# Kernel tuning notes

Measured on AMD Instinct MI355X. Metric: run time of the kernel, lower is better.

The kernel has to match this reference:

```python
import jax, jax.numpy as jnp
import numpy as np
from jax import lax

WINDOW_SIZE = 11
SIGMA = 1.5
LEVELS = 5
WEIGHTS = jnp.array([0.0448, 0.2856, 0.3001, 0.2363, 0.1333], dtype=jnp.float32)


def _make_window(ws, channel):
    # 1D gaussian, sigma=1.5, normalized; outer product -> 2D window, tiled per channel
    x = jnp.arange(ws, dtype=jnp.float32) - ws // 2
    g = jnp.exp(-(x * x) / (2.0 * SIGMA * SIGMA))
    g = g / g.sum()
    w2 = jnp.outer(g, g)  # [ws, ws]
    return jnp.broadcast_to(w2[None, None], (channel, 1, ws, ws))


def _dwconv(x, win, channel):
    # depthwise VALID conv, matches F.conv2d(..., padding=0, groups=channel)
    return lax.conv_general_dilated(
        x, win, window_strides=(1, 1), padding='VALID',
        feature_group_count=channel,
        dimension_numbers=('NCHW', 'OIHW', 'NCHW'))


def _ssim_cs(img1, img2):
    # dynamic data range, as in the torch source (L=1 for [0,1) inputs)
    max_val = jnp.where(jnp.max(img1) > 128.0, 255.0, 1.0)
    min_val = jnp.where(jnp.min(img1) < -0.5, -1.0, 0.0)
    L = max_val - min_val

    n, c, h, w = img1.shape
    ws = min(WINDOW_SIZE, h, w)  # static python int
    win = _make_window(ws, c)

    mu1 = _dwconv(img1, win, c)
    mu2 = _dwconv(img2, win, c)
    mu1_sq = mu1 * mu1
    mu2_sq = mu2 * mu2
    mu1_mu2 = mu1 * mu2
    sigma1_sq = _dwconv(img1 * img1, win, c) - mu1_sq
    sigma2_sq = _dwconv(img2 * img2, win, c) - mu2_sq
    sigma12 = _dwconv(img1 * img2, win, c) - mu1_mu2

    C1 = (0.01 * L) ** 2
    C2 = (0.03 * L) ** 2
    v1 = 2.0 * sigma12 + C2
    v2 = sigma1_sq + sigma2_sq + C2
    cs = jnp.mean(v1 / v2)
    ssim_map = (2.0 * mu1_mu2 + C1) * v1 / ((mu1_sq + mu2_sq + C1) * v2)
    return jnp.mean(ssim_map), cs


def _avg_pool2(x):
    # F.avg_pool2d(x, (2,2)): stride 2, no padding (floors odd dims)
    n, c, h, w = x.shape
    x = x[:, :, : (h // 2) * 2, : (w // 2) * 2]
    return x.reshape(n, c, h // 2, 2, w // 2, 2).mean(axis=(3, 5))


def setup_inputs() -> dict:
    key = jax.random.key(0)
    k1, k2 = jax.random.split(key)
    img1 = jax.random.uniform(k1, (16, 3, 512, 512), dtype=jnp.float32)
    img2 = jax.random.uniform(k2, (16, 3, 512, 512), dtype=jnp.float32)
    return {"img1": img1, "img2": img2}


def reference(img1, img2):
    mssim, mcs = [], []
    for _ in range(LEVELS):  # fixed 5-level pyramid, shapes shrink each level
        s, c = _ssim_cs(img1, img2)
        mssim.append(s)
        mcs.append(c)
        img1 = _avg_pool2(img1)
        img2 = _avg_pool2(img2)
    mssim = (jnp.stack(mssim) + 1.0) / 2.0  # normalize=True
    mcs = (jnp.stack(mcs) + 1.0) / 2.0
    pow1 = mcs ** WEIGHTS
    pow2 = mssim ** WEIGHTS
    # NOTE: faithful to source: prod over (pow1[:-1] * pow2[-1]) broadcasts pow2[-1]
    return jnp.prod(pow1[:-1] * pow2[-1])
```

## Files before the change

kernel.cpp:

```cpp
#include <hip/hip_runtime.h>


#define NSLOT 32

typedef float v4  __attribute__((ext_vector_type(4)));
typedef float v2f __attribute__((ext_vector_type(2)));

__device__ __forceinline__ float frcp(float x) { return __builtin_amdgcn_rcpf(x); }

template<int TROWS, int NTHR, int MINW>
__global__ __launch_bounds__(NTHR, MINW) void ssim_tile_kernel(
    const float* __restrict__ img1, const float* __restrict__ img2,
    float* __restrict__ ds1, float* __restrict__ ds2,
    int H, int do_ds, float* __restrict__ acc)
{
    constexpr int HR    = TROWS + 10;
    constexpr int OPT   = TROWS * 32 / NTHR;
    constexpr int PITCH = 33;
    constexpr int NW    = NTHR / 64;

    const float GW[11] = {0.00102840f, 0.00759877f, 0.03600070f, 0.10936069f,
                          0.21300636f, 0.26601172f, 0.21300636f, 0.10936069f,
                          0.03600070f, 0.00759877f, 0.00102840f};
    const float C1 = 1e-4f, C2 = 9e-4f;

    __shared__ v4 hb[HR * PITCH];
    __shared__ float red[2 * NW];

    const int tid  = threadIdx.x;
    const int nc   = blockIdx.z;
    const int tx0  = blockIdx.x * 32;
    const int ty0  = blockIdx.y * TROWS;
    const int outHW = H - 10;
    const float* p1 = img1 + (size_t)nc * H * H;
    const float* p2 = img2 + (size_t)nc * H * H;

    if (do_ds) {
        const int H2 = H >> 1;
        #pragma unroll
        for (int t = tid; t < 16 * (TROWS / 2); t += NTHR) {
            int r = t >> 4, cdd = t & 15;
            int iy = ty0 + 2 * r, ix = tx0 + 2 * cdd;
            if (iy + 1 < H) {
                v2f a0 = *(const v2f*)(p1 + (size_t)iy * H + ix);
                v2f a1 = *(const v2f*)(p1 + (size_t)(iy + 1) * H + ix);
                v2f b0 = *(const v2f*)(p2 + (size_t)iy * H + ix);
                v2f b1 = *(const v2f*)(p2 + (size_t)(iy + 1) * H + ix);
                size_t o = (size_t)nc * H2 * H2
                         + (size_t)((ty0 >> 1) + r) * H2 + ((tx0 >> 1) + cdd);
                ds1[o] = 0.25f * ((a0.x + a0.y) + (a1.x + a1.y));
                ds2[o] = 0.25f * ((b0.x + b0.y) + (b1.x + b1.y));
            }
        }
    }

    for (int task = tid; task < HR * 8; task += NTHR) {
        const int r  = task >> 3, cg = task & 7;
        const int gr = ty0 + r;
        const int c0 = tx0 + cg * 4;
        v4 hs = 0.f, hd = 0.f, hss = 0.f, hdd = 0.f;
        if (gr < H) {
            float s[16], d[16];
            if (c0 + 16 <= H) {
                const float* pa = p1 + (size_t)gr * H + c0;
                const float* pb = p2 + (size_t)gr * H + c0;
                #pragma unroll
                for (int q = 0; q < 4; ++q) {
                    v4 va = *(const v4*)(pa + 4 * q);
                    v4 vb = *(const v4*)(pb + 4 * q);
                    v4 sv = va + vb, dv = va - vb;
                    s[4*q+0] = sv.x; s[4*q+1] = sv.y; s[4*q+2] = sv.z; s[4*q+3] = sv.w;
                    d[4*q+0] = dv.x; d[4*q+1] = dv.y; d[4*q+2] = dv.z; d[4*q+3] = dv.w;
                }
            } else {
                #pragma unroll
                for (int q = 0; q < 16; ++q) {
                    int cc = c0 + q;
                    float a = (cc < H) ? p1[(size_t)gr * H + cc] : 0.f;
                    float b = (cc < H) ? p2[(size_t)gr * H + cc] : 0.f;
                    s[q] = a + b; d[q] = a - b;
                }
            }
            #pragma unroll
            for (int j = 0; j < 11; ++j) {
                float w = GW[j];
                v4 sv = {s[j], s[j+1], s[j+2], s[j+3]};
                v4 dv = {d[j], d[j+1], d[j+2], d[j+3]};
                v4 ws = w * sv, wd = w * dv;
                hs += ws; hd += wd; hss += ws * sv; hdd += wd * dv;
            }
        }
        v4* row = &hb[r * PITCH + cg * 4];
        row[0] = (v4){hs.x, hd.x, hss.x, hdd.x};
        row[1] = (v4){hs.y, hd.y, hss.y, hdd.y};
        row[2] = (v4){hs.z, hd.z, hss.z, hdd.z};
        row[3] = (v4){hs.w, hd.w, hss.w, hdd.w};
    }
    __syncthreads();

    const int col  = tid & 31;
    const int row0 = (tid >> 5) * OPT;
    const float colm = (tx0 + col < outHW) ? 1.f : 0.f;
    v4 A[OPT];
    #pragma unroll
    for (int k = 0; k < OPT; ++k) A[k] = 0.f;

    #pragma unroll
    for (int r = 0; r < OPT + 10; ++r) {
        v4 h = hb[(row0 + r) * PITCH + col];
        #pragma unroll
        for (int k = 0; k < OPT; ++k) {
            const int j = r - k;
            if (j >= 0 && j < 11) A[k] += GW[j] * h;
        }
    }

    float ssim_t = 0.f, cs_t = 0.f;
    #pragma unroll
    for (int k = 0; k < OPT; ++k) {
        float mask = colm * ((ty0 + row0 + k < outHW) ? 1.f : 0.f);
        float mu_s = A[k].x, mu_d = A[k].y;
        float P = mu_s * mu_s, Q = mu_d * mu_d;
        float U = A[k].z - P, V = A[k].w - Q;
        float v1 = 0.5f * (U - V) + C2;
        float v2 = 0.5f * (U + V) + C2;
        float n1 = 0.5f * (P - Q) + C1;
        float d1 = 0.5f * (P + Q) + C1;
        float csv = v1 * frcp(v2);
        float ssv = n1 * csv * frcp(d1);
        cs_t   += mask * csv;
        ssim_t += mask * ssv;
    }

    #pragma unroll
    for (int off = 32; off > 0; off >>= 1) {
        ssim_t += __shfl_down(ssim_t, off);
        cs_t   += __shfl_down(cs_t, off);
    }
    int wave = tid >> 6, lane = tid & 63;
    if (lane == 0) { red[wave] = ssim_t; red[NW + wave] = cs_t; }
    __syncthreads();
    if (tid == 0) {
        float s = 0.f, c2s = 0.f;
        #pragma unroll
        for (int w = 0; w < NW; ++w) { s += red[w]; c2s += red[NW + w]; }
        int slot = (blockIdx.x + blockIdx.y * 5 + blockIdx.z * 11) & (NSLOT - 1);
        atomicAdd(&acc[slot], s);
        atomicAdd(&acc[NSLOT + slot], c2s);
    }
}

__global__ void finalize_kernel(const float* __restrict__ acc, float* __restrict__ out)
{
    if (threadIdx.x == 0 && blockIdx.x == 0) {
        const float w[5] = {0.0448f, 0.2856f, 0.3001f, 0.2363f, 0.1333f};
        float ms[5], mc[5];
        for (int l = 0; l < 5; ++l) {
            float s = 0.f, c = 0.f;
            for (int k = 0; k < NSLOT; ++k) {
                s += acc[2 * NSLOT * l + k];
                c += acc[2 * NSLOT * l + NSLOT + k];
            }
            int oh = (512 >> l) - 10;
            float cnt = 48.f * (float)oh * (float)oh;
            ms[l] = (s / cnt + 1.f) * 0.5f;
            mc[l] = (c / cnt + 1.f) * 0.5f;
        }
        float p2 = powf(ms[4], w[4]);
        float r = 1.f;
        for (int i = 0; i < 4; ++i) r *= powf(mc[i], w[i]) * p2;
        out[0] = r;
    }
}

extern "C" void kernel_launch(void* const* d_in, const int* in_sizes, int n_in,
                              void* d_out, int out_size, void* d_ws, size_t ws_size,
                              hipStream_t stream)
{
    const float* img1 = (const float*)d_in[0];
    const float* img2 = (const float*)d_in[1];
    float* out = (float*)d_out;
    float* ws  = (float*)d_ws;

    float* acc = ws;
    size_t off = 512;

    const float* buf1[5];
    const float* buf2[5];
    float* wbuf1[5];
    float* wbuf2[5];
    buf1[0] = img1; buf2[0] = img2;
    for (int l = 1; l < 5; ++l) {
        int Hl = 512 >> l;
        size_t sz = (size_t)48 * Hl * Hl;
        wbuf1[l] = ws + off; off += sz;
        wbuf2[l] = ws + off; off += sz;
        buf1[l] = wbuf1[l];
        buf2[l] = wbuf2[l];
    }

    hipMemsetAsync(acc, 0, 5 * 2 * NSLOT * sizeof(float), stream);

    const int Hs[5] = {512, 256, 128, 64, 32};
    const int Ts[5] = {64, 64, 32, 16, 16};

    for (int l = 0; l < 5; ++l) {
        int H = Hs[l], T = Ts[l];
        int outH = H - 10;
        int ctiles = (outH + 31) / 32;
        int rtiles = (outH + T - 1) / T;
        dim3 grid(ctiles, rtiles, 48);
        float* d1 = l < 4 ? wbuf1[l + 1] : nullptr;
        float* d2 = l < 4 ? wbuf2[l + 1] : nullptr;
        int dd = l < 4 ? 1 : 0;
        float* a = acc + 2 * NSLOT * l;
        if (T == 64)
            ssim_tile_kernel<64, 512, 8><<<grid, 512, 0, stream>>>(buf1[l], buf2[l], d1, d2, H, dd, a);
        else if (T == 32)
            ssim_tile_kernel<32, 256, 7><<<grid, 256, 0, stream>>>(buf1[l], buf2[l], d1, d2, H, dd, a);
        else
            ssim_tile_kernel<16, 256, 8><<<grid, 256, 0, stream>>>(buf1[l], buf2[l], d1, d2, H, dd, a);
    }

    finalize_kernel<<<1, 64, 0, stream>>>(acc, out);
}
```

Before: 242.9 us.

## Build full pyramid in level-0 kernel and merge coarse levels into one launch

The level-0 kernel now computes every downsampled pyramid level (2x,4x,8x,16x) straight from the full-resolution input tile, and levels 1-4 run as one flattened tail kernel instead of four separate launches. Atomics and the memset are replaced by per-block partial sums that a 512-thread finalize kernel reduces. This removes launch overhead and serialization across the small coarse levels, and drops atomic contention. In exchange, the level-0 blocks do extra uncoalesced recursive pooling reads, and the coarse levels now run at 512 threads with small tiles, which may leave many threads idle.

```diff
diff --git a/kernel.cpp b/kernel.cpp
--- a/kernel.cpp
+++ b/kernel.cpp
@@ -1,18 +1,32 @@
 #include <hip/hip_runtime.h>
 
 
-#define NSLOT 32
+#define NTHR 512
 
 typedef float v4  __attribute__((ext_vector_type(4)));
 typedef float v2f __attribute__((ext_vector_type(2)));
 
 __device__ __forceinline__ float frcp(float x) { return __builtin_amdgcn_rcpf(x); }
 
-template<int TROWS, int NTHR, int MINW>
-__global__ __launch_bounds__(NTHR, MINW) void ssim_tile_kernel(
-    const float* __restrict__ img1, const float* __restrict__ img2,
-    float* __restrict__ ds1, float* __restrict__ ds2,
-    int H, int do_ds, float* __restrict__ acc)
+template<int L>
+__device__ __forceinline__ float poolv(const float* __restrict__ p, int H, int iy, int ix)
+{
+    if constexpr (L == 1) {
+        const float* r0 = p + (size_t)iy * H + ix;
+        const float* r1 = r0 + H;
+        return 0.25f * ((r0[0] + r0[1]) + (r1[0] + r1[1]));
+    } else {
+        constexpr int s = 1 << (L - 1);
+        return 0.25f * ((poolv<L-1>(p, H, iy, ix)     + poolv<L-1>(p, H, iy, ix + s))
+                      + (poolv<L-1>(p, H, iy + s, ix) + poolv<L-1>(p, H, iy + s, ix + s)));
+    }
+}
+
+template<int TROWS>
+__device__ void ssim_tile(const float* __restrict__ p1, const float* __restrict__ p2,
+                          int H, int tx0, int ty0,
+                          v4* hb, float* red,
+                          float* __restrict__ partS, float* __restrict__ partC)
 {
     constexpr int HR    = TROWS + 10;
     constexpr int OPT   = TROWS * 32 / NTHR;
@@ -24,40 +38,13 @@
                           0.03600070f, 0.00759877f, 0.00102840f};
     const float C1 = 1e-4f, C2 = 9e-4f;
 
-    __shared__ v4 hb[HR * PITCH];
-    __shared__ float red[2 * NW];
-
-    const int tid  = threadIdx.x;
-    const int nc   = blockIdx.z;
-    const int tx0  = blockIdx.x * 32;
-    const int ty0  = blockIdx.y * TROWS;
+    const int tid   = threadIdx.x;
     const int outHW = H - 10;
-    const float* p1 = img1 + (size_t)nc * H * H;
-    const float* p2 = img2 + (size_t)nc * H * H;
-
-    if (do_ds) {
-        const int H2 = H >> 1;
-        #pragma unroll
-        for (int t = tid; t < 16 * (TROWS / 2); t += NTHR) {
-            int r = t >> 4, cdd = t & 15;
-            int iy = ty0 + 2 * r, ix = tx0 + 2 * cdd;
-            if (iy + 1 < H) {
-                v2f a0 = *(const v2f*)(p1 + (size_t)iy * H + ix);
-                v2f a1 = *(const v2f*)(p1 + (size_t)(iy + 1) * H + ix);
-                v2f b0 = *(const v2f*)(p2 + (size_t)iy * H + ix);
-                v2f b1 = *(const v2f*)(p2 + (size_t)(iy + 1) * H + ix);
-                size_t o = (size_t)nc * H2 * H2
-                         + (size_t)((ty0 >> 1) + r) * H2 + ((tx0 >> 1) + cdd);
-                ds1[o] = 0.25f * ((a0.x + a0.y) + (a1.x + a1.y));
-                ds2[o] = 0.25f * ((b0.x + b0.y) + (b1.x + b1.y));
-            }
-        }
-    }
 
     for (int task = tid; task < HR * 8; task += NTHR) {
-        const int r  = task >> 3, cg = task & 7;
+        const int r  = task >> 3, cg2 = task & 7;
         const int gr = ty0 + r;
-        const int c0 = tx0 + cg * 4;
+        const int c0 = tx0 + cg2 * 4;
         v4 hs = 0.f, hd = 0.f, hss = 0.f, hdd = 0.f;
         if (gr < H) {
             float s[16], d[16];
@@ -86,11 +73,11 @@
                 float w = GW[j];
                 v4 sv = {s[j], s[j+1], s[j+2], s[j+3]};
                 v4 dv = {d[j], d[j+1], d[j+2], d[j+3]};
-                v4 ws = w * sv, wd = w * dv;
-                hs += ws; hd += wd; hss += ws * sv; hdd += wd * dv;
+                v4 wsv = w * sv, wdv = w * dv;
+                hs += wsv; hd += wdv; hss += wsv * sv; hdd += wdv * dv;
             }
         }
-        v4* row = &hb[r * PITCH + cg * 4];
+        v4* row = &hb[r * PITCH + cg2 * 4];
         row[0] = (v4){hs.x, hd.x, hss.x, hdd.x};
         row[1] = (v4){hs.y, hd.y, hss.y, hdd.y};
         row[2] = (v4){hs.z, hd.z, hss.z, hdd.z};
@@ -141,30 +128,143 @@
     if (lane == 0) { red[wave] = ssim_t; red[NW + wave] = cs_t; }
     __syncthreads();
     if (tid == 0) {
-        float s = 0.f, c2s = 0.f;
+        float s = 0.f, c = 0.f;
         #pragma unroll
-        for (int w = 0; w < NW; ++w) { s += red[w]; c2s += red[NW + w]; }
-        int slot = (blockIdx.x + blockIdx.y * 5 + blockIdx.z * 11) & (NSLOT - 1);
-        atomicAdd(&acc[slot], s);
-        atomicAdd(&acc[NSLOT + slot], c2s);
-    }
-}
-
-__global__ void finalize_kernel(const float* __restrict__ acc, float* __restrict__ out)
-{
-    if (threadIdx.x == 0 && blockIdx.x == 0) {
+        for (int w = 0; w < NW; ++w) { s += red[w]; c += red[NW + w]; }
+        partS[0] = s; partC[0] = c;
+    }
+}
+
+__global__ __launch_bounds__(NTHR, 8) void l0_kernel(
+    const float* __restrict__ img1, const float* __restrict__ img2,
+    float* __restrict__ x1a, float* __restrict__ x1b,
+    float* __restrict__ x2a, float* __restrict__ x2b,
+    float* __restrict__ x3a, float* __restrict__ x3b,
+    float* __restrict__ x4a, float* __restrict__ x4b,
+    float* __restrict__ accS, float* __restrict__ accC)
+{
+    __shared__ v4 hb[74 * 33];
+    __shared__ float red[16];
+
+    const int tid = threadIdx.x;
+    const int nc  = blockIdx.z;
+    const int tx0 = blockIdx.x * 32;
+    const int ty0 = blockIdx.y * 64;
+    const int H   = 512;
+    const float* p1 = img1 + (size_t)nc * H * H;
+    const float* p2 = img2 + (size_t)nc * H * H;
+
+    for (int t = tid; t < 680; t += NTHR) {
+        if (t < 512) {
+            int r = t >> 4, c = t & 15;
+            int iy = ty0 + 2 * r, ix = tx0 + 2 * c;
+            size_t o = (size_t)nc * 256 * 256 + (size_t)((ty0 >> 1) + r) * 256 + ((tx0 >> 1) + c);
+            x1a[o] = poolv<1>(p1, H, iy, ix);
+            x1b[o] = poolv<1>(p2, H, iy, ix);
+        } else if (t < 640) {
+            int t2 = t - 512; int r = t2 >> 3, c = t2 & 7;
+            int iy = ty0 + 4 * r, ix = tx0 + 4 * c;
+            size_t o = (size_t)nc * 128 * 128 + (size_t)((ty0 >> 2) + r) * 128 + ((tx0 >> 2) + c);
+            x2a[o] = poolv<2>(p1, H, iy, ix);
+            x2b[o] = poolv<2>(p2, H, iy, ix);
+        } else if (t < 672) {
+            int t3 = t - 640; int r = t3 >> 2, c = t3 & 3;
+            int iy = ty0 + 8 * r, ix = tx0 + 8 * c;
+            size_t o = (size_t)nc * 64 * 64 + (size_t)((ty0 >> 3) + r) * 64 + ((tx0 >> 3) + c);
+            x3a[o] = poolv<3>(p1, H, iy, ix);
+            x3b[o] = poolv<3>(p2, H, iy, ix);
+        } else {
+            int t4 = t - 672; int r = t4 >> 1, c = t4 & 1;
+            int iy = ty0 + 16 * r, ix = tx0 + 16 * c;
+            size_t o = (size_t)nc * 32 * 32 + (size_t)((ty0 >> 4) + r) * 32 + ((tx0 >> 4) + c);
+            x4a[o] = poolv<4>(p1, H, iy, ix);
+            x4b[o] = poolv<4>(p2, H, iy, ix);
+        }
+    }
+
+    int fb = (int)blockIdx.x + (int)gridDim.x * ((int)blockIdx.y + (int)gridDim.y * (int)blockIdx.z);
+    ssim_tile<64>(p1, p2, H, tx0, ty0, hb, red, accS + fb, accC + fb);
+}
+
+__global__ __launch_bounds__(NTHR, 8) void tail_kernel(
+    const float* __restrict__ x1a, const float* __restrict__ x1b,
+    const float* __restrict__ x2a, const float* __restrict__ x2b,
+    const float* __restrict__ x3a, const float* __restrict__ x3b,
+    const float* __restrict__ x4a, const float* __restrict__ x4b,
+    float* __restrict__ accTS, float* __restrict__ accTC)
+{
+    __shared__ v4 hb[74 * 33];
+    __shared__ float red[16];
+
+    const int b = (int)blockIdx.x;
+    if (b < 1536) {
+        const int H = 256, ct = 8, rt = 4;
+        int cx = b % ct, rem = b / ct, cy = rem % rt, nc = rem / rt;
+        const float* p1 = x1a + (size_t)nc * H * H;
+        const float* p2 = x1b + (size_t)nc * H * H;
+        ssim_tile<64>(p1, p2, H, cx * 32, cy * 64, hb, red, accTS + b, accTC + b);
+    } else if (b < 2304) {
+        const int H = 128, ct = 4, rt = 4;
+        int lb = b - 1536;
+        int cx = lb % ct, rem = lb / ct, cy = rem % rt, nc = rem / rt;
+        const float* p1 = x2a + (size_t)nc * H * H;
+        const float* p2 = x2b + (size_t)nc * H * H;
+        ssim_tile<32>(p1, p2, H, cx * 32, cy * 32, hb, red, accTS + b, accTC + b);
+    } else if (b < 2688) {
+        const int H = 64, ct = 2, rt = 4;
+        int lb = b - 2304;
+        int cx = lb % ct, rem = lb / ct, cy = rem % rt, nc = rem / rt;
+        const float* p1 = x3a + (size_t)nc * H * H;
+        const float* p2 = x3b + (size_t)nc * H * H;
+        ssim_tile<16>(p1, p2, H, cx * 32, cy * 16, hb, red, accTS + b, accTC + b);
+    } else {
+        const int H = 32, ct = 1, rt = 2;
+        int lb = b - 2688;
+        int cx = lb % ct, rem = lb / ct, cy = rem % rt, nc = rem / rt;
+        const float* p1 = x4a + (size_t)nc * H * H;
+        const float* p2 = x4b + (size_t)nc * H * H;
+        ssim_tile<16>(p1, p2, H, cx * 32, cy * 16, hb, red, accTS + b, accTC + b);
+    }
+}
+
+__global__ void finalize_kernel(const float* __restrict__ acc0S, const float* __restrict__ acc0C,
+                                const float* __restrict__ accTS, const float* __restrict__ accTC,
+                                float* __restrict__ out)
+{
+    __shared__ float sm[10];
+    __shared__ float wred[8];
+    const int tid  = (int)threadIdx.x;
+    const int wave = tid >> 6, lane = tid & 63;
+    const int st[5] = {0, 0, 1536, 2304, 2688};
+    const int en[5] = {6144, 1536, 2304, 2688, 2784};
+
+    for (int srs = 0; srs < 10; ++srs) {
+        int l = srs >> 1;
+        const float* base = (srs & 1) ? (l == 0 ? acc0C : accTC)
+                                      : (l == 0 ? acc0S : accTS);
+        float p = 0.f;
+        for (int i = st[l] + tid; i < en[l]; i += NTHR) p += base[i];
+        #pragma unroll
+        for (int o = 32; o > 0; o >>= 1) p += __shfl_down(p, o);
+        if (lane == 0) wred[wave] = p;
+        __syncthreads();
+        if (tid == 0) {
+            float t = 0.f;
+            #pragma unroll
+            for (int w = 0; w < 8; ++w) t += wred[w];
+            sm[srs] = t;
+        }
+        __syncthreads();
+    }
+
+    if (tid == 0) {
         const float w[5] = {0.0448f, 0.2856f, 0.3001f, 0.2363f, 0.1333f};
         float ms[5], mc[5];
         for (int l = 0; l < 5; ++l) {
-            float s = 0.f, c = 0.f;
-            for (int k = 0; k < NSLOT; ++k) {
-                s += acc[2 * NSLOT * l + k];
-                c += acc[2 * NSLOT * l + NSLOT + k];
-            }
             int oh = (512 >> l) - 10;
             float cnt = 48.f * (float)oh * (float)oh;
-            ms[l] = (s / cnt + 1.f) * 0.5f;
-            mc[l] = (c / cnt + 1.f) * 0.5f;
+            ms[l] = (sm[2 * l] / cnt + 1.f) * 0.5f;
+            mc[l] = (sm[2 * l + 1] / cnt + 1.f) * 0.5f;
         }
         float p2 = powf(ms[4], w[4]);
         float r = 1.f;
@@ -177,50 +277,31 @@
                               void* d_out, int out_size, void* d_ws, size_t ws_size,
                               hipStream_t stream)
 {
+    (void)in_sizes; (void)n_in; (void)out_size; (void)ws_size;
     const float* img1 = (const float*)d_in[0];
     const float* img2 = (const float*)d_in[1];
     float* out = (float*)d_out;
     float* ws  = (float*)d_ws;
 
-    float* acc = ws;
-    size_t off = 512;
-
-    const float* buf1[5];
-    const float* buf2[5];
-    float* wbuf1[5];
-    float* wbuf2[5];
-    buf1[0] = img1; buf2[0] = img2;
-    for (int l = 1; l < 5; ++l) {
-        int Hl = 512 >> l;
-        size_t sz = (size_t)48 * Hl * Hl;
-        wbuf1[l] = ws + off; off += sz;
-        wbuf2[l] = ws + off; off += sz;
-        buf1[l] = wbuf1[l];
-        buf2[l] = wbuf2[l];
-    }
-
-    hipMemsetAsync(acc, 0, 5 * 2 * NSLOT * sizeof(float), stream);
-
-    const int Hs[5] = {512, 256, 128, 64, 32};
-    const int Ts[5] = {64, 64, 32, 16, 16};
-
-    for (int l = 0; l < 5; ++l) {
-        int H = Hs[l], T = Ts[l];
-        int outH = H - 10;
-        int ctiles = (outH + 31) / 32;
-        int rtiles = (outH + T - 1) / T;
-        dim3 grid(ctiles, rtiles, 48);
-        float* d1 = l < 4 ? wbuf1[l + 1] : nullptr;
-        float* d2 = l < 4 ? wbuf2[l + 1] : nullptr;
-        int dd = l < 4 ? 1 : 0;
-        float* a = acc + 2 * NSLOT * l;
-        if (T == 64)
-            ssim_tile_kernel<64, 512, 8><<<grid, 512, 0, stream>>>(buf1[l], buf2[l], d1, d2, H, dd, a);
-        else if (T == 32)
-            ssim_tile_kernel<32, 256, 7><<<grid, 256, 0, stream>>>(buf1[l], buf2[l], d1, d2, H, dd, a);
-        else
-            ssim_tile_kernel<16, 256, 8><<<grid, 256, 0, stream>>>(buf1[l], buf2[l], d1, d2, H, dd, a);
-    }
-
-    finalize_kernel<<<1, 64, 0, stream>>>(acc, out);
-}
+    float* acc0S = ws;
+    float* acc0C = acc0S + 6144;
+    float* accTS = acc0C + 6144;
+    float* accTC = accTS + 2784;
+    float* bufs  = accTC + 2784;
+    float* x1a = bufs;
+    float* x1b = x1a + (size_t)48 * 256 * 256;
+    float* x2a = x1b + (size_t)48 * 256 * 256;
+    float* x2b = x2a + (size_t)48 * 128 * 128;
+    float* x3a = x2b + (size_t)48 * 128 * 128;
+    float* x3b = x3a + (size_t)48 * 64 * 64;
+    float* x4a = x3b + (size_t)48 * 64 * 64;
+    float* x4b = x4a + (size_t)48 * 32 * 32;
+
+    l0_kernel<<<dim3(16, 8, 48), NTHR, 0, stream>>>(
+        img1, img2, x1a, x1b, x2a, x2b, x3a, x3b, x4a, x4b, acc0S, acc0C);
+
+    tail_kernel<<<dim3(2784), NTHR, 0, stream>>>(
+        x1a, x1b, x2a, x2b, x3a, x3b, x4a, x4b, accTS, accTC);
+
+    finalize_kernel<<<1, NTHR, 0, stream>>>(acc0S, acc0C, accTS, accTC, out);
+}
```

Result: slower. 521.7 us (+114.8%).
